# Optimization experiments

Measured on AMD Instinct MI355X. Metric: run time of the kernel, lower is better.

The kernel has to match this reference:

```python
import jax, jax.numpy as jnp
import numpy as np

NUM_PID = 5532
QUEUE_SIZE = 5000
DIM = 256
BATCH = 4096


def _l2norm(x, axis=-1, eps=1e-12):
    return x / jnp.maximum(jnp.linalg.norm(x, axis=axis, keepdims=True), eps)


def setup_inputs() -> dict:
    key = jax.random.key(0)
    k1, k2, k3, k4, k5 = jax.random.split(key, 5)
    inputs = _l2norm(jax.random.normal(k1, (BATCH, DIM), dtype=jnp.float32))
    # targets in [-1, NUM_PID): -1 marks unlabeled identities (go to the circular queue)
    targets = jax.random.randint(k2, (BATCH,), -1, NUM_PID)
    gt_flag = jax.random.bernoulli(k3, 0.5, (BATCH,))
    lut = _l2norm(jax.random.normal(k4, (NUM_PID, DIM), dtype=jnp.float32))
    queue = _l2norm(jax.random.normal(k5, (QUEUE_SIZE, DIM), dtype=jnp.float32))
    return {"inputs": inputs, "targets": targets, "gt_flag": gt_flag, "lut": lut, "queue": queue}


def reference(inputs, targets, gt_flag, lut, queue):
    # MatchFunction.forward (lut.dim()==2 path): similarity of features against
    # the labeled lookup table and the unlabeled circular queue.
    outputs_labeled = inputs @ lut.T            # [B, num_pid]
    outputs_unlabeled = inputs @ queue.T        # [B, Q]
    return jnp.concatenate([outputs_labeled, outputs_unlabeled], axis=1)
```

## Files before the change

### kernel.cpp

```cpp
#include <hip/hip_runtime.h>
#include <hip/hip_bf16.h>
#include <stdint.h>


#define M_DIM 4096
#define K_DIM 256
#define N_LUT 5532
#define N_Q   5000
#define N_DIM (N_LUT + N_Q)
#define BN    256
#define NT_N  42
#define N_PAD (NT_N * 256)
#define NSTRIP 6

typedef _Float16 f16x8 __attribute__((ext_vector_type(8)));
typedef float f32x4 __attribute__((ext_vector_type(4)));

__device__ __forceinline__ unsigned short f2h(float f) {
  union { _Float16 h; unsigned short u; } v;
  v.h = (_Float16)f;
  return v.u;
}

__global__ __launch_bounds__(256) void convert_kernel(
    const float* __restrict__ inp, const float* __restrict__ lut,
    const float* __restrict__ que, unsigned short* __restrict__ Abf,
    unsigned short* __restrict__ Bbf) {
  const int AV = M_DIM * K_DIM / 4;
  int i = blockIdx.x * 256 + threadIdx.x;
  float4 x;
  unsigned short* dst;
  if (i < AV) {
    x = ((const float4*)inp)[i];
    dst = Abf + i * 4;
  } else {
    int e = (i - AV) * 4;
    int row = e >> 8;
    int col = e & 255;
    if (row < N_LUT)
      x = *(const float4*)(lut + (size_t)row * K_DIM + col);
    else if (row < N_DIM)
      x = *(const float4*)(que + (size_t)(row - N_LUT) * K_DIM + col);
    else
      x = make_float4(0.f, 0.f, 0.f, 0.f);
    dst = Bbf + e;
  }
  ushort4 o;
  o.x = f2h(x.x); o.y = f2h(x.y); o.z = f2h(x.z); o.w = f2h(x.w);
  *(ushort4*)dst = o;
}

#define GLDS16(gsrc, ldst)                                                  \
  __builtin_amdgcn_global_load_lds(                                         \
      (__attribute__((address_space(1))) void*)(gsrc),                      \
      (__attribute__((address_space(3))) void*)(ldst), 16, 0, 0)

__global__ __launch_bounds__(512, 2) void gemm_kernel(
    const unsigned short* __restrict__ A, const unsigned short* __restrict__ B,
    float* __restrict__ C) {
  __shared__ __align__(16) unsigned short As[2][32 * 256];

  const int t = threadIdx.x;
  const int lane = t & 63;
  const int wave = t >> 6;

  {
  }
  const int bid = blockIdx.x;
  const int xcd = bid & 7, idx = bid >> 3;
  const int wg =
      ((xcd < 4) ? xcd * 32 : 128 + (xcd - 4) * 31) + idx;
  const int s = wg / NT_N;
  const int bn = wg % NT_N;
  const int bcol = bn * BN;
  const bool fullN = (bcol + BN <= N_DIM);
  const int csub = 21 + (s >= 4 ? 1 : 0);
  const int sub0 = 21 * s + (s >= 5 ? 1 : 0);
  const int row0 = sub0 * 32;

  const int lr = lane & 15;
  const int rsw = lane & 7;
  const int cq = lane >> 4;
  const int cc4 = cq * 4;

  f16x8 breg[2][8];
#pragma unroll
  for (int j = 0; j < 2; ++j) {
    const unsigned short* brow =
        B + (size_t)(bcol + wave * 32 + j * 16 + lr) * K_DIM + cq * 8;
#pragma unroll
    for (int ks = 0; ks < 8; ++ks)
      breg[j][ks] = *(const f16x8*)(brow + ks * 32);
  }

  const int srow = t >> 5;
  const int scs = (((t & 31) ^ (srow & 7)) * 8);
  const unsigned short* gaBase0 = A + (size_t)(row0 + srow) * K_DIM + scs;
  const int ldsRound = wave * 2 * 256;

#define STAGE_A(buf, sub)                                                    \
  do {                                                                       \
    _Pragma("unroll") for (int r = 0; r < 2; ++r)                            \
      GLDS16(gaBase0 + ((size_t)(sub) * 32 + r * 16) * K_DIM,                \
             As[buf] + r * 16 * 256 + ldsRound);                             \
  } while (0)

  STAGE_A(0, 0);
  __syncthreads();

  int cur = 0;
#pragma unroll 1
  for (int sub = 0; sub < csub; ++sub) {
    if (sub + 1 < csub)
      STAGE_A(cur ^ 1, sub + 1);
    __builtin_amdgcn_sched_barrier(0);

    f32x4 acc[2][2] = {};
#pragma unroll
    for (int ks = 0; ks < 8; ++ks) {
      const int ch = (ks * 4 + cq) ^ rsw;
      f16x8 a[2];
#pragma unroll
      for (int i = 0; i < 2; ++i)
        a[i] = *(const f16x8*)&As[cur][(i * 16 + lr) * 256 + ch * 8];
#pragma unroll
      for (int i = 0; i < 2; ++i)
#pragma unroll
        for (int j = 0; j < 2; ++j)
          acc[i][j] = __builtin_amdgcn_mfma_f32_16x16x32_f16(breg[j][ks], a[i],
                                                             acc[i][j], 0, 0, 0);
    }

#pragma unroll
    for (int i = 0; i < 2; ++i) {
      size_t rowBase = (size_t)(row0 + sub * 32 + i * 16 + lr) * N_DIM;
#pragma unroll
      for (int j = 0; j < 2; ++j) {
        int col = bcol + wave * 32 + j * 16 + cc4;
        if (col < N_DIM)
          *(f32x4*)&C[rowBase + col] = acc[i][j];
      }
    }

    if (sub + 1 < csub) {
      if (fullN)
        asm volatile("s_waitcnt vmcnt(4)" ::: "memory");
      else
        asm volatile("s_waitcnt vmcnt(0)" ::: "memory");
      asm volatile("s_barrier" ::: "memory");
    }
    cur ^= 1;
  }
#undef STAGE_A
}

extern "C" void kernel_launch(void* const* d_in, const int* in_sizes, int n_in,
                              void* d_out, int out_size, void* d_ws, size_t ws_size,
                              hipStream_t stream) {
  const float* inp = (const float*)d_in[0];
  const float* lut = (const float*)d_in[3];
  const float* que = (const float*)d_in[4];
  float* C = (float*)d_out;

  unsigned short* Abf = (unsigned short*)d_ws;
  unsigned short* Bbf = Abf + (size_t)M_DIM * K_DIM;

  const int conv_blocks = (M_DIM * K_DIM / 4 + N_PAD * K_DIM / 4) / 256;
  convert_kernel<<<conv_blocks, 256, 0, stream>>>(inp, lut, que, Abf, Bbf);

  gemm_kernel<<<NSTRIP * NT_N, 512, 0, stream>>>(Abf, Bbf, C);
}
```

Baseline: 47.51 us.

## Fuse LUT/queue fp16 conversion into GEMM B-register load

```diff
diff --git a/kernel.cpp b/kernel.cpp
--- a/kernel.cpp
+++ b/kernel.cpp
@@ -10,44 +10,20 @@
 #define N_DIM (N_LUT + N_Q)
 #define BN    256
 #define NT_N  42
-#define N_PAD (NT_N * 256)
 #define NSTRIP 6
 
 typedef _Float16 f16x8 __attribute__((ext_vector_type(8)));
 typedef float f32x4 __attribute__((ext_vector_type(4)));
 
-__device__ __forceinline__ unsigned short f2h(float f) {
-  union { _Float16 h; unsigned short u; } v;
-  v.h = (_Float16)f;
-  return v.u;
-}
-
 __global__ __launch_bounds__(256) void convert_kernel(
-    const float* __restrict__ inp, const float* __restrict__ lut,
-    const float* __restrict__ que, unsigned short* __restrict__ Abf,
-    unsigned short* __restrict__ Bbf) {
-  const int AV = M_DIM * K_DIM / 4;
+    const float* __restrict__ inp, unsigned short* __restrict__ Abf) {
   int i = blockIdx.x * 256 + threadIdx.x;
-  float4 x;
-  unsigned short* dst;
-  if (i < AV) {
-    x = ((const float4*)inp)[i];
-    dst = Abf + i * 4;
-  } else {
-    int e = (i - AV) * 4;
-    int row = e >> 8;
-    int col = e & 255;
-    if (row < N_LUT)
-      x = *(const float4*)(lut + (size_t)row * K_DIM + col);
-    else if (row < N_DIM)
-      x = *(const float4*)(que + (size_t)(row - N_LUT) * K_DIM + col);
-    else
-      x = make_float4(0.f, 0.f, 0.f, 0.f);
-    dst = Bbf + e;
-  }
-  ushort4 o;
-  o.x = f2h(x.x); o.y = f2h(x.y); o.z = f2h(x.z); o.w = f2h(x.w);
-  *(ushort4*)dst = o;
+  float4 x = ((const float4*)inp)[i];
+  union { _Float16 h; unsigned short u; } a, b, c, d;
+  a.h = (_Float16)x.x; b.h = (_Float16)x.y;
+  c.h = (_Float16)x.z; d.h = (_Float16)x.w;
+  ushort4 o; o.x = a.u; o.y = b.u; o.z = c.u; o.w = d.u;
+  *(ushort4*)(Abf + i * 4) = o;
 }
 
 #define GLDS16(gsrc, ldst)                                                  \
@@ -56,20 +32,17 @@
       (__attribute__((address_space(3))) void*)(ldst), 16, 0, 0)
 
 __global__ __launch_bounds__(512, 2) void gemm_kernel(
-    const unsigned short* __restrict__ A, const unsigned short* __restrict__ B,
-    float* __restrict__ C) {
+    const unsigned short* __restrict__ A, const float* __restrict__ lut,
+    const float* __restrict__ que, float* __restrict__ C) {
   __shared__ __align__(16) unsigned short As[2][32 * 256];
 
   const int t = threadIdx.x;
   const int lane = t & 63;
   const int wave = t >> 6;
 
-  {
-  }
   const int bid = blockIdx.x;
   const int xcd = bid & 7, idx = bid >> 3;
-  const int wg =
-      ((xcd < 4) ? xcd * 32 : 128 + (xcd - 4) * 31) + idx;
+  const int wg = ((xcd < 4) ? xcd * 32 : 128 + (xcd - 4) * 31) + idx;
   const int s = wg / NT_N;
   const int bn = wg % NT_N;
   const int bcol = bn * BN;
@@ -82,16 +55,6 @@
   const int rsw = lane & 7;
   const int cq = lane >> 4;
   const int cc4 = cq * 4;
-
-  f16x8 breg[2][8];
-#pragma unroll
-  for (int j = 0; j < 2; ++j) {
-    const unsigned short* brow =
-        B + (size_t)(bcol + wave * 32 + j * 16 + lr) * K_DIM + cq * 8;
-#pragma unroll
-    for (int ks = 0; ks < 8; ++ks)
-      breg[j][ks] = *(const f16x8*)(brow + ks * 32);
-  }
 
   const int srow = t >> 5;
   const int scs = (((t & 31) ^ (srow & 7)) * 8);
@@ -106,6 +69,33 @@
   } while (0)
 
   STAGE_A(0, 0);
+
+  f16x8 breg[2][8];
+#pragma unroll
+  for (int j = 0; j < 2; ++j) {
+    const int row = bcol + wave * 32 + j * 16 + lr;
+    const bool valid = row < N_DIM;
+    const float* src = (row < N_LUT) ? (lut + (size_t)row * K_DIM)
+                      : valid        ? (que + (size_t)(row - N_LUT) * K_DIM)
+                                     : lut;
+#pragma unroll
+    for (int ks = 0; ks < 8; ++ks) {
+      const float* p = src + ks * 32 + cq * 8;
+      f32x4 lo = *(const f32x4*)p;
+      f32x4 hi = *(const f32x4*)(p + 4);
+      if (!valid) {
+        lo = (f32x4){0.f, 0.f, 0.f, 0.f};
+        hi = (f32x4){0.f, 0.f, 0.f, 0.f};
+      }
+      f16x8 v;
+      v[0] = (_Float16)lo[0]; v[1] = (_Float16)lo[1];
+      v[2] = (_Float16)lo[2]; v[3] = (_Float16)lo[3];
+      v[4] = (_Float16)hi[0]; v[5] = (_Float16)hi[1];
+      v[6] = (_Float16)hi[2]; v[7] = (_Float16)hi[3];
+      breg[j][ks] = v;
+    }
+  }
+
   __syncthreads();
 
   int cur = 0;
@@ -163,10 +153,9 @@
   float* C = (float*)d_out;
 
   unsigned short* Abf = (unsigned short*)d_ws;
-  unsigned short* Bbf = Abf + (size_t)M_DIM * K_DIM;
 
-  const int conv_blocks = (M_DIM * K_DIM / 4 + N_PAD * K_DIM / 4) / 256;
-  convert_kernel<<<conv_blocks, 256, 0, stream>>>(inp, lut, que, Abf, Bbf);
+  const int conv_blocks = M_DIM * K_DIM / 4 / 256;
+  convert_kernel<<<conv_blocks, 256, 0, stream>>>(inp, Abf);
 
-  gemm_kernel<<<NSTRIP * NT_N, 512, 0, stream>>>(Abf, Bbf, C);
+  gemm_kernel<<<NSTRIP * NT_N, 512, 0, stream>>>(Abf, lut, que, C);
 }
```

Result: slower. 50.23 us (+5.7%).
